# Performance work log

Measured on AMD Instinct MI355X. Metric: run time of the kernel, lower is better.

The kernel has to match this reference:

```python
import jax, jax.numpy as jnp
import numpy as np

C = 256
B, H, W = 2, 64, 64


def conv1x1(x, Wt, b):
    # x: [B, Cin, H, W], Wt: [Cout, Cin], b: [Cout]
    return jnp.einsum('bchw,oc->bohw', x, Wt) + b[None, :, None, None]


def setup_inputs() -> dict:
    key = jax.random.key(0)
    ks = jax.random.split(key, 16)
    s = 0.02
    d = {
        'input1': jax.random.normal(ks[0], (B, C, H, W), jnp.float32),
        'input2': jax.random.normal(ks[1], (B, C, H, W), jnp.float32),
        'Wq1': jax.random.normal(ks[2], (C // 4, C), jnp.float32) * s,
        'bq1': jnp.zeros((C // 4,), jnp.float32),
        'Wk1': jax.random.normal(ks[3], (C // 2, C), jnp.float32) * s,
        'bk1': jnp.zeros((C // 2,), jnp.float32),
        'Wv1': jax.random.normal(ks[4], (C, C), jnp.float32) * s,
        'bv1': jnp.zeros((C,), jnp.float32),
        'Wq2': jax.random.normal(ks[5], (C // 4, C), jnp.float32) * s,
        'bq2': jnp.zeros((C // 4,), jnp.float32),
        'Wk2': jax.random.normal(ks[6], (C // 2, C), jnp.float32) * s,
        'bk2': jnp.zeros((C // 2,), jnp.float32),
        'Wv2': jax.random.normal(ks[7], (C, C), jnp.float32) * s,
        'bv2': jnp.zeros((C,), jnp.float32),
        'gamma': jax.random.normal(ks[8], (1,), jnp.float32) * 0.1,
    }
    return d


def reference(input1, input2, Wq1, bq1, Wk1, bk1, Wv1, bv1,
              Wq2, bq2, Wk2, bk2, Wv2, bv2, gamma):
    b, c, h, w = input1.shape
    hw = h * w
    q1 = conv1x1(input1, Wq1, bq1)                      # [B, C/4, H, W]
    k1 = conv1x1(input1, Wk1, bk1).reshape(b, -1, hw)   # [B, C/2, HW]
    v1 = conv1x1(input1, Wv1, bv1).reshape(b, -1, hw)   # [B, C,   HW]
    q2 = conv1x1(input2, Wq2, bq2)
    k2 = conv1x1(input2, Wk2, bk2).reshape(b, -1, hw)
    v2 = conv1x1(input2, Wv2, bv2).reshape(b, -1, hw)

    # cat on new dim 2 then 'b c t h w -> b (c t) h w' interleaves q1/q2 channels
    q = jnp.stack([q1, q2], axis=2).reshape(b, c // 2, hw)  # [B, C/2, HW]
    q = q.transpose(0, 2, 1)                                # [B, HW, C/2]

    a1 = jax.nn.softmax(jnp.einsum('bnc,bcm->bnm', q, k1), axis=-1)  # [B, HW, HW]
    out1 = jnp.einsum('bcm,bnm->bcn', v1, a1).reshape(b, c, h, w)
    out1 = gamma[0] * out1 + input1

    a2 = jax.nn.softmax(jnp.einsum('bnc,bcm->bnm', q, k2), axis=-1)
    out2 = jnp.einsum('bcm,bnm->bcn', v2, a2).reshape(b, c, h, w)
    out2 = gamma[0] * out2 + input2
    return (out1, out2)
```

## Files before the change

### kernel.cpp

```cpp
#include <hip/hip_runtime.h>

typedef __attribute__((ext_vector_type(8)))  short bf16x8;
typedef __attribute__((ext_vector_type(4)))  float f32x4;
typedef __attribute__((ext_vector_type(16))) float f32x16;
typedef __attribute__((ext_vector_type(8)))  unsigned short u16x8;

#define HW 4096
#define CDIM 256

#if __has_builtin(__builtin_amdgcn_exp2f)
#define EXP2(x) __builtin_amdgcn_exp2f(x)
#else
#define EXP2(x) exp2f(x)
#endif

__device__ __forceinline__ unsigned short f2bf(float f) {
    union { float f; unsigned u; } v; v.f = f;
    unsigned r = v.u + 0x7fffu + ((v.u >> 16) & 1u);
    return (unsigned short)(r >> 16);
}
__device__ __forceinline__ float bf2f(unsigned short u) {
    union { unsigned u; float f; } v; v.u = ((unsigned)u) << 16;
    return v.f;
}
__device__ __forceinline__ unsigned pk2(float hi, float lo) {
    union { float f; unsigned u; } a, b; a.f = hi; b.f = lo;
    return __builtin_amdgcn_perm(a.u, b.u, 0x07060302u);
}
__device__ __forceinline__ void gl_lds16(const void* g, void* l) {
    __builtin_amdgcn_global_load_lds(
        (const __attribute__((address_space(1))) unsigned int*)(unsigned long long)g,
        (__attribute__((address_space(3))) unsigned int*)(unsigned int)(unsigned long long)l,
        16, 0, 0);
}

__global__ __launch_bounds__(256) void wpack_kernel(
    const float* __restrict__ Wq1, const float* __restrict__ Wk1,
    const float* __restrict__ Wv1, const float* __restrict__ Wq2,
    const float* __restrict__ Wk2, const float* __restrict__ Wv2,
    unsigned short* __restrict__ Wpk)
{
    const int i  = blockIdx.x * 256 + threadIdx.x;
    const int c4 = i & 63;
    const int r6 = i >> 6;
    const int inp = r6 / 448;
    const int o   = r6 - inp * 448;
    const float* src;
    int orow;
    if (o < 64)       { src = inp ? Wq2 : Wq1; orow = o; }
    else if (o < 192) { src = inp ? Wk2 : Wk1; orow = o - 64; }
    else              { src = inp ? Wv2 : Wv1; orow = o - 192; }
    const float4 v = *(const float4*)(src + (size_t)orow * CDIM + c4 * 4);
    uint2 pkd; pkd.x = pk2(v.y, v.x); pkd.y = pk2(v.w, v.z);
    ((uint2*)Wpk)[i] = pkd;
}

__global__ __launch_bounds__(256) void proj_kernel(
    const float* __restrict__ in1, const float* __restrict__ in2,
    const float* __restrict__ bq1, const float* __restrict__ bk1,
    const float* __restrict__ bv1, const float* __restrict__ bq2,
    const float* __restrict__ bk2, const float* __restrict__ bv2,
    const unsigned short* __restrict__ Wpk,
    unsigned short* __restrict__ Qg, unsigned short* __restrict__ Kg,
    unsigned short* __restrict__ Vg)
{
    __shared__ unsigned xb[32 * 128];

    const int bid   = blockIdx.x;
    const int ntile = bid & 127;
    const int inp   = (bid >> 7) & 1;
    const int b     = bid >> 8;

    const float* X  = (inp ? in2 : in1) + (size_t)b * CDIM * HW;
    const float* bq = inp ? bq2 : bq1;
    const float* bk = inp ? bk2 : bk1;
    const float* bv = inp ? bv2 : bv1;
    const unsigned short* Wb = Wpk + (size_t)inp * 448 * CDIM;

    const int tid  = threadIdx.x;
    const int lane = tid & 63;
    const int w    = tid >> 6;
    const int l15  = lane & 15, quad = lane >> 4;
    const int n0   = ntile * 32;

#pragma unroll
    for (int t = 0; t < 4; ++t) {
        const int idx = t * 256 + tid;
        const int cp  = idx >> 3;
        const int n4  = idx & 7;
        const float* p0 = X + (size_t)(cp * 2) * HW + n0 + n4 * 4;
        const float4 a = *(const float4*)p0;
        const float4 bb = *(const float4*)(p0 + HW);
        const float av[4] = {a.x, a.y, a.z, a.w};
        const float bv4[4] = {bb.x, bb.y, bb.z, bb.w};
#pragma unroll
        for (int r = 0; r < 4; ++r) {
            const int n = n4 * 4 + r;
            xb[n * 128 + (((cp >> 2) ^ (n & 7)) << 2) + (cp & 3)] = pk2(bv4[r], av[r]);
        }
    }
    __syncthreads();

    f32x4 acc[7][2];
#pragma unroll
    for (int i = 0; i < 7; ++i)
#pragma unroll
        for (int j = 0; j < 2; ++j) acc[i][j] = (f32x4){0.f, 0.f, 0.f, 0.f};

#pragma unroll
    for (int kk = 0; kk < 8; ++kk) {
        bf16x8 xf[2];
#pragma unroll
        for (int ns = 0; ns < 2; ++ns) {
            const int nrow = ns * 16 + l15;
            xf[ns] = *(const bf16x8*)&xb[nrow * 128 + (((kk * 4 + quad) ^ (nrow & 7)) << 2)];
        }
#pragma unroll
        for (int os = 0; os < 7; ++os) {
            const int ob = w * 7 + os;
            const int og = ob * 16 + l15;
            const bf16x8 wf = *(const bf16x8*)(Wb + (size_t)og * CDIM + kk * 32 + quad * 8);
            if (ob < 12) {
#pragma unroll
                for (int ns = 0; ns < 2; ++ns)
                    acc[os][ns] = __builtin_amdgcn_mfma_f32_16x16x32_bf16(xf[ns], wf, acc[os][ns], 0, 0, 0);
            } else {
#pragma unroll
                for (int ns = 0; ns < 2; ++ns)
                    acc[os][ns] = __builtin_amdgcn_mfma_f32_16x16x32_bf16(wf, xf[ns], acc[os][ns], 0, 0, 0);
            }
        }
    }

    const size_t qbase = (size_t)b * HW * 128;
    const size_t kbase = (size_t)(b * 2 + inp) * HW * 128;
    const size_t vbase = (size_t)(b * 2 + inp) * (size_t)CDIM * HW;
#pragma unroll
    for (int os = 0; os < 7; ++os) {
        const int ob = w * 7 + os;
        if (ob < 4) {
            const int o = ob * 16 + l15;
            const float bb = bq[o];
#pragma unroll
            for (int ns = 0; ns < 2; ++ns) {
                const f32x4 d = acc[os][ns];
#pragma unroll
                for (int r = 0; r < 4; ++r) {
                    const int n = n0 + ns * 16 + quad * 4 + r;
                    Qg[qbase + (size_t)n * 128 + 2 * o + inp] =
                        f2bf((d[r] + bb) * 1.4426950408889634f);
                }
            }
        } else if (ob < 12) {
            const int c = (ob - 4) * 16 + l15;
            const float bb = bk[c];
#pragma unroll
            for (int ns = 0; ns < 2; ++ns) {
                const f32x4 d = acc[os][ns];
#pragma unroll
                for (int r = 0; r < 4; ++r) {
                    const int n = n0 + ns * 16 + quad * 4 + r;
                    Kg[kbase + (size_t)n * 128 + c] = f2bf(d[r] + bb);
                }
            }
        } else {
            const int c0 = (ob - 12) * 16 + quad * 4;
#pragma unroll
            for (int ns = 0; ns < 2; ++ns) {
                const f32x4 d = acc[os][ns];
#pragma unroll
                for (int r = 0; r < 4; ++r) {
                    const int n = n0 + ns * 16 + l15;
                    Vg[vbase + (size_t)(c0 + r) * HW + n] = f2bf(d[r] + bv[c0 + r]);
                }
            }
        }
    }
}

__global__ __launch_bounds__(256) void attn_kernel(
    const unsigned short* __restrict__ Qg, const unsigned short* __restrict__ Kg,
    const unsigned short* __restrict__ Vg,
    unsigned short* __restrict__ Op, float* __restrict__ Lp)
{
    __shared__ unsigned short kbuf[2][32 * 16 * 8];
    __shared__ unsigned short vbuf[2][256 * 4 * 8];

    const int bid = blockIdx.x;
    const int set = (bid & 7) >> 1;
    const int att = set & 1, b = set >> 1;
    const int sub = ((bid >> 3) << 1) | (bid & 1);
    const int mh  = sub & 1, qt = sub >> 1;
    const int n0g = qt * 64;
    const int mbase = mh * 2048;
    const int tid = threadIdx.x;
    const int lane = tid & 63, w = tid >> 6;
    const int l31 = lane & 31, h = lane >> 5;
    const int ng = w >> 1, ch = w & 1;

    const unsigned short* Qb = Qg + (size_t)b * HW * 128;
    const unsigned short* Kb = Kg + (size_t)(b * 2 + att) * HW * 128;
    const unsigned short* Vb = Vg + (size_t)(b * 2 + att) * (size_t)CDIM * HW;

    bf16x8 aQ[8];
    {
        const int n = n0g + ng * 32 + l31;
#pragma unroll
        for (int kk = 0; kk < 8; ++kk)
            aQ[kk] = *(const bf16x8*)(Qb + (size_t)n * 128 + kk * 16 + h * 8);
    }

    f32x16 acc[4];
#pragma unroll
    for (int i = 0; i < 4; ++i)
#pragma unroll
        for (int r = 0; r < 16; ++r) acc[i][r] = 0.f;
    float lsum = 0.f;

    const unsigned short* ksrc[2]; unsigned short* kdst[2][2];
    const unsigned short* vsrc[4]; unsigned short* vdst[2][4];
#pragma unroll
    for (int t = 0; t < 2; ++t) {
        const int L = (t * 4 + w) * 64 + lane;
        const int ml = L >> 4, s = L & 15;
        const int g = s ^ (ml & 15);
        ksrc[t] = Kb + (size_t)ml * 128 + g * 8;
        kdst[0][t] = &kbuf[0][L * 8]; kdst[1][t] = &kbuf[1][L * 8];
    }
#pragma unroll
    for (int t = 0; t < 4; ++t) {
        const int L = (t * 4 + w) * 64 + lane;
        const int c = L >> 2, s = L & 3;
        const int g = s ^ ((c >> 2) & 3);
        vsrc[t] = Vb + (size_t)c * HW + g * 8;
        vdst[0][t] = &vbuf[0][L * 8]; vdst[1][t] = &vbuf[1][L * 8];
    }

    auto stage = [&](int mt, int bs) {
        const int m0 = mbase + mt * 32;
#pragma unroll
        for (int t = 0; t < 2; ++t) gl_lds16(ksrc[t] + (size_t)m0 * 128, kdst[bs][t]);
#pragma unroll
        for (int t = 0; t < 4; ++t) gl_lds16(vsrc[t] + m0, vdst[bs][t]);
    };

    stage(0, 0);

    for (int mt = 0; mt < 64; ++mt) {
        __syncthreads();
        if (mt + 1 < 64) stage(mt + 1, (mt + 1) & 1);
        const int cur = mt & 1;

        f32x16 sa, sb;
#pragma unroll
        for (int r = 0; r < 16; ++r) { sa[r] = 0.f; sb[r] = 0.f; }
#pragma unroll
        for (int kk = 0; kk < 4; ++kk) {
            bf16x8 bK = *(const bf16x8*)&kbuf[cur][(l31 * 16 + ((kk * 2 + h) ^ (l31 & 15))) * 8];
            sa = __builtin_amdgcn_mfma_f32_32x32x16_bf16(bK, aQ[kk], sa, 0, 0, 0);
        }
#pragma unroll
        for (int kk = 4; kk < 8; ++kk) {
            bf16x8 bK = *(const bf16x8*)&kbuf[cur][(l31 * 16 + ((kk * 2 + h) ^ (l31 & 15))) * 8];
            sb = __builtin_amdgcn_mfma_f32_32x32x16_bf16(bK, aQ[kk], sb, 0, 0, 0);
        }

        float p[16];
#pragma unroll
        for (int r = 0; r < 16; ++r) {
            p[r] = EXP2(sa[r] + sb[r]);
            lsum += p[r];
        }

        bf16x8 bP[2];
#pragma unroll
        for (int k2 = 0; k2 < 2; ++k2) {
            const float* pp = p + k2 * 8;
            const unsigned a0 = pk2(pp[1], pp[0]);
            const unsigned a1 = pk2(pp[3], pp[2]);
            const unsigned b0 = pk2(pp[5], pp[4]);
            const unsigned b1 = pk2(pp[7], pp[6]);
            auto s0 = __builtin_amdgcn_permlane32_swap(a0, b0, false, false);
            auto s1 = __builtin_amdgcn_permlane32_swap(a1, b1, false, false);
            union { unsigned u[4]; bf16x8 v; } uu;
            uu.u[0] = s0[0];
            uu.u[1] = s1[0];
            uu.u[2] = s0[1];
            uu.u[3] = s1[1];
            bP[k2] = uu.v;
        }

#pragma unroll
        for (int cf = 0; cf < 4; ++cf) {
            const int c = ch * 128 + cf * 32 + l31;
#pragma unroll
            for (int k2 = 0; k2 < 2; ++k2) {
                bf16x8 aV = *(const bf16x8*)&vbuf[cur][(c * 4 + ((k2 * 2 + h) ^ ((c >> 2) & 3))) * 8];
                acc[cf] = __builtin_amdgcn_mfma_f32_32x32x16_bf16(aV, bP[k2], acc[cf], 0, 0, 0);
            }
        }
    }

    const float ltot = lsum + __shfl_xor(lsum, 32, 64);
    const int nn = n0g + ng * 32 + l31;
    if (ch == 0 && h == 0) Lp[(size_t)(mh * 4 + set) * HW + nn] = ltot;

    const size_t obase = (size_t)(mh * 4 + set) * CDIM * HW;
#pragma unroll
    for (int cf = 0; cf < 4; ++cf) {
#pragma unroll
        for (int r = 0; r < 16; ++r) {
            const int c = ch * 128 + cf * 32 + (r & 3) + 8 * (r >> 2) + 4 * h;
            Op[obase + (size_t)c * HW + nn] = f2bf(acc[cf][r]);
        }
    }
}

__global__ __launch_bounds__(256) void combine_kernel(
    const unsigned short* __restrict__ Op, const float* __restrict__ Lp,
    const float* __restrict__ in1, const float* __restrict__ in2,
    const float* __restrict__ gamma_p, float* __restrict__ out)
{
    const size_t i8 = ((size_t)blockIdx.x * 256 + threadIdx.x) * 8;
    const int oset = (int)(i8 >> 20);
    const int att = oset >> 1, b = oset & 1;
    const int pset = b * 2 + att;
    const size_t rem = i8 & 1048575u;
    const int n = (int)(i8 & 4095);

    const u16x8 o0 = *(const u16x8*)(Op + ((size_t)pset << 20) + rem);
    const u16x8 o1 = *(const u16x8*)(Op + ((size_t)pset << 20) + rem + ((size_t)4 << 20));
    const f32x4 la0 = *(const f32x4*)(Lp + (size_t)pset * HW + n);
    const f32x4 la1 = *(const f32x4*)(Lp + (size_t)pset * HW + n + 4);
    const f32x4 lb0 = *(const f32x4*)(Lp + (size_t)(4 + pset) * HW + n);
    const f32x4 lb1 = *(const f32x4*)(Lp + (size_t)(4 + pset) * HW + n + 4);
    const float* inb = (att ? in2 : in1) + (size_t)b * CDIM * HW + rem;
    const float g = *gamma_p;

    const f32x4 iv0 = *(const f32x4*)(inb);
    const f32x4 iv1 = *(const f32x4*)(inb + 4);
    f32x4 r0, r1;
#pragma unroll
    for (int j = 0; j < 4; ++j) {
        const float ov = bf2f((unsigned short)o0[j]) + bf2f((unsigned short)o1[j]);
        r0[j] = g * ov / (la0[j] + lb0[j]) + iv0[j];
    }
#pragma unroll
    for (int j = 0; j < 4; ++j) {
        const float ov = bf2f((unsigned short)o0[j + 4]) + bf2f((unsigned short)o1[j + 4]);
        r1[j] = g * ov / (la1[j] + lb1[j]) + iv1[j];
    }
    *(f32x4*)(out + i8) = r0;
    *(f32x4*)(out + i8 + 4) = r1;
}

extern "C" void kernel_launch(void* const* d_in, const int* in_sizes, int n_in,
                              void* d_out, int out_size, void* d_ws, size_t ws_size,
                              hipStream_t stream) {
    const float* in1 = (const float*)d_in[0];
    const float* in2 = (const float*)d_in[1];
    const float* Wq1 = (const float*)d_in[2];  const float* bq1 = (const float*)d_in[3];
    const float* Wk1 = (const float*)d_in[4];  const float* bk1 = (const float*)d_in[5];
    const float* Wv1 = (const float*)d_in[6];  const float* bv1 = (const float*)d_in[7];
    const float* Wq2 = (const float*)d_in[8];  const float* bq2 = (const float*)d_in[9];
    const float* Wk2 = (const float*)d_in[10]; const float* bk2 = (const float*)d_in[11];
    const float* Wv2 = (const float*)d_in[12]; const float* bv2 = (const float*)d_in[13];
    const float* gamma = (const float*)d_in[14];

    unsigned short* Qg = (unsigned short*)d_ws;
    unsigned short* Kg = Qg + (size_t)2 * HW * 128;
    unsigned short* Vg = Kg + (size_t)4 * HW * 128;
    unsigned short* Op = Vg + (size_t)4 * CDIM * HW;
    float*          Lp = (float*)(Op + (size_t)8 * CDIM * HW);
    unsigned short* Wpk = Op;

    wpack_kernel<<<224, 256, 0, stream>>>(Wq1, Wk1, Wv1, Wq2, Wk2, Wv2, Wpk);
    proj_kernel<<<512, 256, 0, stream>>>(in1, in2, bq1, bk1, bv1, bq2, bk2, bv2,
                                         Wpk, Qg, Kg, Vg);
    attn_kernel<<<512, 256, 0, stream>>>(Qg, Kg, Vg, Op, Lp);
    combine_kernel<<<2048, 256, 0, stream>>>(Op, Lp, in1, in2, gamma, (float*)d_out);
}
```

Measured before the change: 209.6 us.

## Split attention key range into quarters with 128-query tiles per block

The attention kernel now gives each block 128 queries (one 32-row group per wave) and one quarter of the key range, instead of 64 queries and half the keys. Each wave covers all 256 output channels, so every K tile staged in shared memory feeds twice as many query rows. The combine kernel now sums four partial outputs and four partial softmax denominators. The cost is doubled accumulator registers per wave (8 f32x16 tiles) with launch_bounds requesting 2 blocks per CU, plus twice the partial-output workspace and more combine reads.

Result: faster. 179.2 us (-14.5%).

```diff
diff --git a/kernel.cpp b/kernel.cpp
--- a/kernel.cpp
+++ b/kernel.cpp
@@ -178,7 +178,7 @@
     }
 }
 
-__global__ __launch_bounds__(256) void attn_kernel(
+__global__ __launch_bounds__(256, 2) void attn_kernel(
     const unsigned short* __restrict__ Qg, const unsigned short* __restrict__ Kg,
     const unsigned short* __restrict__ Vg,
     unsigned short* __restrict__ Op, float* __restrict__ Lp)
@@ -187,16 +187,15 @@
     __shared__ unsigned short vbuf[2][256 * 4 * 8];
 
     const int bid = blockIdx.x;
-    const int set = (bid & 7) >> 1;
+    const int mq  = bid & 3;
+    const int set = (bid >> 2) & 3;
     const int att = set & 1, b = set >> 1;
-    const int sub = ((bid >> 3) << 1) | (bid & 1);
-    const int mh  = sub & 1, qt = sub >> 1;
-    const int n0g = qt * 64;
-    const int mbase = mh * 2048;
+    const int nt  = bid >> 4;
+    const int n0g = nt * 128;
+    const int mbase = mq * 1024;
     const int tid = threadIdx.x;
     const int lane = tid & 63, w = tid >> 6;
     const int l31 = lane & 31, h = lane >> 5;
-    const int ng = w >> 1, ch = w & 1;
 
     const unsigned short* Qb = Qg + (size_t)b * HW * 128;
     const unsigned short* Kb = Kg + (size_t)(b * 2 + att) * HW * 128;
@@ -204,15 +203,15 @@
 
     bf16x8 aQ[8];
     {
-        const int n = n0g + ng * 32 + l31;
+        const int n = n0g + w * 32 + l31;
 #pragma unroll
         for (int kk = 0; kk < 8; ++kk)
             aQ[kk] = *(const bf16x8*)(Qb + (size_t)n * 128 + kk * 16 + h * 8);
     }
 
-    f32x16 acc[4];
-#pragma unroll
-    for (int i = 0; i < 4; ++i)
+    f32x16 acc[8];
+#pragma unroll
+    for (int i = 0; i < 8; ++i)
 #pragma unroll
         for (int r = 0; r < 16; ++r) acc[i][r] = 0.f;
     float lsum = 0.f;
@@ -246,9 +245,9 @@
 
     stage(0, 0);
 
-    for (int mt = 0; mt < 64; ++mt) {
+    for (int mt = 0; mt < 32; ++mt) {
         __syncthreads();
-        if (mt + 1 < 64) stage(mt + 1, (mt + 1) & 1);
+        if (mt + 1 < 32) stage(mt + 1, (mt + 1) & 1);
         const int cur = mt & 1;
 
         f32x16 sa, sb;
@@ -291,8 +290,8 @@
         }
 
 #pragma unroll
-        for (int cf = 0; cf < 4; ++cf) {
-            const int c = ch * 128 + cf * 32 + l31;
+        for (int cf = 0; cf < 8; ++cf) {
+            const int c = cf * 32 + l31;
 #pragma unroll
             for (int k2 = 0; k2 < 2; ++k2) {
                 bf16x8 aV = *(const bf16x8*)&vbuf[cur][(c * 4 + ((k2 * 2 + h) ^ ((c >> 2) & 3))) * 8];
@@ -302,15 +301,15 @@
     }
 
     const float ltot = lsum + __shfl_xor(lsum, 32, 64);
-    const int nn = n0g + ng * 32 + l31;
-    if (ch == 0 && h == 0) Lp[(size_t)(mh * 4 + set) * HW + nn] = ltot;
-
-    const size_t obase = (size_t)(mh * 4 + set) * CDIM * HW;
-#pragma unroll
-    for (int cf = 0; cf < 4; ++cf) {
+    const int nn = n0g + w * 32 + l31;
+    if (h == 0) Lp[(size_t)(mq * 4 + set) * HW + nn] = ltot;
+
+    const size_t obase = (size_t)(mq * 4 + set) * CDIM * HW;
+#pragma unroll
+    for (int cf = 0; cf < 8; ++cf) {
 #pragma unroll
         for (int r = 0; r < 16; ++r) {
-            const int c = ch * 128 + cf * 32 + (r & 3) + 8 * (r >> 2) + 4 * h;
+            const int c = cf * 32 + (r & 3) + 8 * (r >> 2) + 4 * h;
             Op[obase + (size_t)c * HW + nn] = f2bf(acc[cf][r]);
         }
     }
@@ -328,12 +327,14 @@
     const size_t rem = i8 & 1048575u;
     const int n = (int)(i8 & 4095);
 
-    const u16x8 o0 = *(const u16x8*)(Op + ((size_t)pset << 20) + rem);
-    const u16x8 o1 = *(const u16x8*)(Op + ((size_t)pset << 20) + rem + ((size_t)4 << 20));
-    const f32x4 la0 = *(const f32x4*)(Lp + (size_t)pset * HW + n);
-    const f32x4 la1 = *(const f32x4*)(Lp + (size_t)pset * HW + n + 4);
-    const f32x4 lb0 = *(const f32x4*)(Lp + (size_t)(4 + pset) * HW + n);
-    const f32x4 lb1 = *(const f32x4*)(Lp + (size_t)(4 + pset) * HW + n + 4);
+    u16x8 o[4];
+    f32x4 l0[4], l1[4];
+#pragma unroll
+    for (int mq = 0; mq < 4; ++mq) {
+        o[mq]  = *(const u16x8*)(Op + ((size_t)(mq * 4 + pset) << 20) + rem);
+        l0[mq] = *(const f32x4*)(Lp + (size_t)(mq * 4 + pset) * HW + n);
+        l1[mq] = *(const f32x4*)(Lp + (size_t)(mq * 4 + pset) * HW + n + 4);
+    }
     const float* inb = (att ? in2 : in1) + (size_t)b * CDIM * HW + rem;
     const float g = *gamma_p;
 
@@ -342,13 +343,23 @@
     f32x4 r0, r1;
 #pragma unroll
     for (int j = 0; j < 4; ++j) {
-        const float ov = bf2f((unsigned short)o0[j]) + bf2f((unsigned short)o1[j]);
-        r0[j] = g * ov / (la0[j] + lb0[j]) + iv0[j];
+        float ov = 0.f, ld = 0.f;
+#pragma unroll
+        for (int mq = 0; mq < 4; ++mq) {
+            ov += bf2f((unsigned short)o[mq][j]);
+            ld += l0[mq][j];
+        }
+        r0[j] = g * ov / ld + iv0[j];
     }
 #pragma unroll
     for (int j = 0; j < 4; ++j) {
-        const float ov = bf2f((unsigned short)o0[j + 4]) + bf2f((unsigned short)o1[j + 4]);
-        r1[j] = g * ov / (la1[j] + lb1[j]) + iv1[j];
+        float ov = 0.f, ld = 0.f;
+#pragma unroll
+        for (int mq = 0; mq < 4; ++mq) {
+            ov += bf2f((unsigned short)o[mq][j + 4]);
+            ld += l1[mq][j];
+        }
+        r1[j] = g * ov / ld + iv1[j];
     }
     *(f32x4*)(out + i8) = r0;
     *(f32x4*)(out + i8 + 4) = r1;
@@ -371,7 +382,7 @@
     unsigned short* Kg = Qg + (size_t)2 * HW * 128;
     unsigned short* Vg = Kg + (size_t)4 * HW * 128;
     unsigned short* Op = Vg + (size_t)4 * CDIM * HW;
-    float*          Lp = (float*)(Op + (size_t)8 * CDIM * HW);
+    float*          Lp = (float*)(Op + (size_t)16 * CDIM * HW);
     unsigned short* Wpk = Op;
 
     wpack_kernel<<<224, 256, 0, stream>>>(Wq1, Wk1, Wv1, Wq2, Wk2, Wv2, Wpk);
```
